# Optimization experiments

Hardware: AMD Instinct MI355X
Metric: run time of the kernel (lower is better)

Reference implementation:

```python
import jax, jax.numpy as jnp
import numpy as np

EMBED = 1024
HEADS = 16


def setup_inputs() -> dict:
    key = jax.random.key(0)
    ks = jax.random.split(key, 12)
    B, S, E = 8, 4096, EMBED
    img = jax.random.normal(ks[0], (B, S, E), dtype=jnp.float32)
    text = jax.random.normal(ks[1], (B, 1, E), dtype=jnp.float32)
    scale = 0.02
    W_kit = jax.random.normal(ks[2], (E, E), dtype=jnp.float32) * scale
    b_kit = jnp.zeros((E,), jnp.float32)
    W_vit = jax.random.normal(ks[3], (E, E), dtype=jnp.float32) * scale
    b_vit = jnp.zeros((E,), jnp.float32)
    W_kti = jax.random.normal(ks[4], (E, E), dtype=jnp.float32) * scale
    b_kti = jnp.zeros((E,), jnp.float32)
    W_vti = jax.random.normal(ks[5], (E, E), dtype=jnp.float32) * scale
    b_vti = jnp.zeros((E,), jnp.float32)
    W_out = jax.random.normal(ks[6], (E, E), dtype=jnp.float32) * scale
    b_out = jnp.zeros((E,), jnp.float32)
    return {
        "img": img, "text": text,
        "W_kit": W_kit, "b_kit": b_kit,
        "W_vit": W_vit, "b_vit": b_vit,
        "W_kti": W_kti, "b_kti": b_kti,
        "W_vti": W_vti, "b_vti": b_vti,
        "W_out": W_out, "b_out": b_out,
        "num_heads": HEADS,
    }


def reference(img, text, W_kit, b_kit, W_vit, b_vit, W_kti, b_kti,
              W_vti, b_vti, W_out, b_out, num_heads):
    B, S, E = img.shape
    H = num_heads
    D = E // H
    inv_sqrt_d = 1.0 / jnp.sqrt(jnp.asarray(D, img.dtype))

    # Projections (torch Linear with weights stored as [in, out] here)
    k_it = (img @ W_kit + b_kit).reshape(B, S, H, D)   # img_to_text_keys
    v_it = (img @ W_vit + b_vit).reshape(B, S, H, D)   # img_to_text_values
    k_ti = (text @ W_kti + b_kti).reshape(B, 1, H, D)  # text_to_img_keys
    v_ti = (text @ W_vti + b_vti).reshape(B, 1, H, D)  # text_to_img_values

    # text.repeat(1, S, 1).view(B, S, H, D): text has seq len 1
    t_keys = jnp.broadcast_to(text, (B, S, E)).reshape(B, S, H, D)
    img_keys = img.reshape(B, S, H, D)

    # NOTE: the original einsums attend over the HEADS axis (q,k = H),
    # with n = sequence position. Attention matrices are [B, S, H, H].
    img_att = jax.nn.softmax(
        jnp.einsum('bnqd,bnkd->bnqk', t_keys, k_it) * inv_sqrt_d, axis=-1)
    # torch einsum broadcasts the size-1 'n' dim of k_ti; do it explicitly
    k_ti_b = jnp.broadcast_to(k_ti, (B, S, H, D))
    v_ti_b = jnp.broadcast_to(v_ti, (B, S, H, D))
    text_att = jax.nn.softmax(
        jnp.einsum('bnqd,bnkd->bnqk', img_keys, k_ti_b) * inv_sqrt_d, axis=-1)

    img_out = jnp.einsum('bnql,bnld->bnqd', img_att, v_it).reshape(B, S, E)
    text_out = jnp.einsum('bnql,bnld->bnqd', text_att, v_ti_b).reshape(B, S, E)

    out = jnp.concatenate((img_out, text_out), axis=1)  # [B, 2S, E]
    return out @ W_out + b_out
```

## Files before the change

kernel.cpp:

```cpp
#include <hip/hip_runtime.h>
#include <stdint.h>

#define E_DIM 1024
#define SEQ 4096
#define BATCH 8

typedef unsigned short u16;
typedef __attribute__((ext_vector_type(8))) short bf16x8;
typedef __attribute__((ext_vector_type(4))) float f32x4;

static __device__ __forceinline__ float bf2f(u16 u){
  union { unsigned u; float f; } x; x.u = ((unsigned)u) << 16; return x.f;
}
static __device__ __forceinline__ u16 f2bf(float f){
  union { float f; unsigned u; } x; x.f = f;
  unsigned r = (x.u + 0x7fffu + ((x.u >> 16) & 1u)) >> 16;
  return (u16)r;
}
static __device__ __forceinline__ void lds_fence(){
  __asm__ volatile("s_waitcnt lgkmcnt(0)" ::: "memory");
}
static __device__ __forceinline__ void gload_lds16(const u16* g, u16* l){
  __builtin_amdgcn_global_load_lds(
      (const __attribute__((address_space(1))) unsigned int*)g,
      (__attribute__((address_space(3))) unsigned int*)l, 16, 0, 0);
}

__global__ __launch_bounds__(256) void conv_f2b(
    const float* __restrict__ src, u16* __restrict__ dst)
{
  size_t i = ((size_t)blockIdx.x * 256 + threadIdx.x) * 8;
  float4 a = *(const float4*)(src + i);
  float4 b = *(const float4*)(src + i + 4);
  u16 tmp[8] __attribute__((aligned(16)));
  tmp[0] = f2bf(a.x); tmp[1] = f2bf(a.y); tmp[2] = f2bf(a.z); tmp[3] = f2bf(a.w);
  tmp[4] = f2bf(b.x); tmp[5] = f2bf(b.y); tmp[6] = f2bf(b.z); tmp[7] = f2bf(b.w);
  *(uint4*)(dst + i) = *(const uint4*)tmp;
}

__global__ __launch_bounds__(256) void prep_transpose(
    const float* __restrict__ Wkit, const float* __restrict__ Wvit,
    const float* __restrict__ Wout, u16* __restrict__ Wt_kv,
    u16* __restrict__ Wt_out)
{
  __shared__ __align__(16) float sT[64][65];
  int m = blockIdx.y;
  const float* src = (m == 0) ? Wkit : (m == 1) ? Wvit : Wout;
  u16* dst = (m == 0) ? Wt_kv : (m == 1) ? (Wt_kv + 1024 * 1024) : Wt_out;
  int tile = blockIdx.x;
  int r0 = (tile & 15) * 64;
  int c0 = (tile >> 4) * 64;
  int t = threadIdx.x;
  #pragma unroll
  for (int it = 0; it < 4; ++it){
    int idx = t + it * 256;
    int r = idx >> 4, cq = idx & 15;
    float4 v = *(const float4*)(src + (size_t)(r0 + r) * 1024 + c0 + cq * 4);
    sT[r][cq * 4 + 0] = v.x; sT[r][cq * 4 + 1] = v.y;
    sT[r][cq * 4 + 2] = v.z; sT[r][cq * 4 + 3] = v.w;
  }
  __syncthreads();
  #pragma unroll
  for (int it = 0; it < 2; ++it){
    int idx = t + it * 256;
    int c = idx >> 3, rb = idx & 7;
    u16 tmp[8] __attribute__((aligned(16)));
    #pragma unroll
    for (int j = 0; j < 8; ++j) tmp[j] = f2bf(sT[rb * 8 + j][c]);
    *(uint4*)(dst + (size_t)(c0 + c) * 1024 + r0 + rb * 8) = *(const uint4*)tmp;
  }
}

__global__ __launch_bounds__(256) void prep_bias(
    const float* __restrict__ bkit, const float* __restrict__ bvit,
    float* __restrict__ bkv)
{
  int i = blockIdx.x * 256 + threadIdx.x;
  bkv[i] = (i < 1024) ? bkit[i] : bvit[i - 1024];
}

__global__ __launch_bounds__(1024) void prep_ti(
    const float* __restrict__ text,
    const float* __restrict__ Wk, const float* __restrict__ bk,
    const float* __restrict__ Wv, const float* __restrict__ bv,
    u16* __restrict__ kti, u16* __restrict__ vtiT)
{
  __shared__ __align__(16) float sT[1024];
  int b = blockIdx.x;
  int m = blockIdx.y;
  int e = threadIdx.x;
  const float* W = (m == 0) ? Wk : Wv;
  const float* bias = (m == 0) ? bk : bv;
  sT[e] = text[(size_t)b * 1024 + e];
  __syncthreads();
  float acc = bias[e];
  #pragma unroll 8
  for (int k = 0; k < 1024; ++k)
    acc += sT[k] * W[(size_t)k * 1024 + e];
  u16 r = f2bf(acc);
  if (m == 0) kti[(size_t)b * 1024 + e] = r;
  else {
    int kh = e >> 6, d = e & 63;
    vtiT[(size_t)b * 1024 + d * 16 + kh] = r;
  }
}

template <typename CT, bool VPERM>
__global__ __launch_bounds__(256, 2) void gemm_bt(
    const u16* __restrict__ A, const u16* __restrict__ Bt,
    const float* __restrict__ bias, CT* __restrict__ C,
    int n_tiles, int G, int ldc)
{
  __shared__ __align__(16) u16 sA[128 * 64];
  __shared__ __align__(16) u16 sB[128 * 64];
  int nwg = gridDim.x;
  int cpx = nwg >> 3;
  int bid = (blockIdx.x & 7) * cpx + (blockIdx.x >> 3);
  int gb = G * n_tiles;
  int g = bid / gb;
  int r = bid - g * gb;
  int mt = g * G + (r % G);
  int nt = r / G;
  int m0 = mt * 128, n0 = nt * 128;
  int tid = threadIdx.x;
  int w = tid >> 6, lane = tid & 63;
  int wm = w & 1, wn = w >> 1;
  int quad = lane >> 4, l15 = lane & 15;
  f32x4 acc[4][4];
  #pragma unroll
  for (int i = 0; i < 4; ++i)
    #pragma unroll
    for (int j = 0; j < 4; ++j)
      acc[i][j] = (f32x4){0.f, 0.f, 0.f, 0.f};
  const u16* Abase = A + (size_t)m0 * 1024;
  const u16* Bbase = Bt + (size_t)n0 * 1024;
  int srow = lane >> 3;
  int scol = (lane & 7) * 8;
  for (int kt = 0; kt < 16; ++kt){
    int k0 = kt * 64;
    #pragma unroll
    for (int i = 0; i < 4; ++i){
      int c = i * 4 + w;
      int grow = c * 8 + srow;
      gload_lds16(Abase + (size_t)grow * 1024 + k0 + scol, sA + c * 512);
      gload_lds16(Bbase + (size_t)grow * 1024 + k0 + scol, sB + c * 512);
    }
    __syncthreads();
    #pragma unroll
    for (int ks = 0; ks < 2; ++ks){
      bf16x8 af[4], bfr[4];
      #pragma unroll
      for (int mi = 0; mi < 4; ++mi){
        int rt = wm * 64 + mi * 16 + l15;
        af[mi] = *(const bf16x8*)(sA + rt * 64 + (ks * 4 + quad) * 8);
      }
      #pragma unroll
      for (int ni = 0; ni < 4; ++ni){
        int rt = wn * 64 + ni * 16 + l15;
        bfr[ni] = *(const bf16x8*)(sB + rt * 64 + (ks * 4 + quad) * 8);
      }
      #pragma unroll
      for (int mi = 0; mi < 4; ++mi)
        #pragma unroll
        for (int ni = 0; ni < 4; ++ni)
          acc[mi][ni] = __builtin_amdgcn_mfma_f32_16x16x32_bf16(
              af[mi], bfr[ni], acc[mi][ni], 0, 0, 0);
    }
    __syncthreads();
  }
  #pragma unroll
  for (int ni = 0; ni < 4; ++ni){
    int col = n0 + wn * 64 + ni * 16 + l15;
    float bv = bias[col];
    #pragma unroll
    for (int mi = 0; mi < 4; ++mi){
      int row0 = m0 + wm * 64 + mi * 16 + quad * 4;
      #pragma unroll
      for (int rg = 0; rg < 4; ++rg){
        float v = acc[mi][ni][rg] + bv;
        size_t cidx;
        if constexpr (VPERM) {
          if (n0 >= 1024) {
            int c2 = col - 1024;
            cidx = (size_t)(row0 + rg) * ldc + 1024 + (c2 & 63) * 16 + (c2 >> 6);
          } else {
            cidx = (size_t)(row0 + rg) * ldc + col;
          }
        } else {
          cidx = (size_t)(row0 + rg) * ldc + col;
        }
        if constexpr (sizeof(CT) == 2)
          C[cidx] = (CT)f2bf(v);
        else
          C[cidx] = (CT)v;
      }
    }
  }
}

static __device__ __forceinline__ void softmax16(const f32x4& s, float* p){
  #pragma unroll
  for (int g = 0; g < 4; ++g){
    float v = s[g] * 0.125f;
    float m = v;
    m = fmaxf(m, __shfl_xor(m, 1, 16));
    m = fmaxf(m, __shfl_xor(m, 2, 16));
    m = fmaxf(m, __shfl_xor(m, 4, 16));
    m = fmaxf(m, __shfl_xor(m, 8, 16));
    float e = __expf(v - m);
    float t = e;
    t += __shfl_xor(t, 1, 16);
    t += __shfl_xor(t, 2, 16);
    t += __shfl_xor(t, 4, 16);
    t += __shfl_xor(t, 8, 16);
    p[g] = e / t;
  }
}

__global__ __launch_bounds__(256) void attn_kernel(
    const u16* __restrict__ img, const u16* __restrict__ text,
    const u16* __restrict__ kv, const u16* __restrict__ kti,
    const u16* __restrict__ vtiT, u16* __restrict__ attn, int b0)
{
  __shared__ __align__(16) u16 sP[4][16 * 32];
  int tid = threadIdx.x;
  int w = tid >> 6, lane = tid & 63;
  int quad = lane >> 4, l15 = lane & 15;
  u16* sPw = sP[w];
  const f32x4 fz = {0.f, 0.f, 0.f, 0.f};
  const bf16x8 bz = {0, 0, 0, 0, 0, 0, 0, 0};
  int rloc = blockIdx.x * 4 + w;
  int bb = rloc >> 12;
  int n = rloc & 4095;
  int b = b0 + bb;
  const u16* xrow = img + ((size_t)b * SEQ + n) * E_DIM;
  const u16* trow = text + (size_t)b * E_DIM;
  const u16* kvrow = kv + (size_t)rloc * 2048;
  u16* dst1 = attn + ((size_t)bb * 8192 + n) * E_DIM;
  u16* dst2 = attn + ((size_t)bb * 8192 + 4096 + n) * E_DIM;

  {
    f32x4 s = fz;
    #pragma unroll
    for (int ks = 0; ks < 2; ++ks){
      bf16x8 a  = *(const bf16x8*)(trow  + l15 * 64 + ks * 32 + quad * 8);
      bf16x8 bk = *(const bf16x8*)(kvrow + l15 * 64 + ks * 32 + quad * 8);
      s = __builtin_amdgcn_mfma_f32_16x16x32_bf16(a, bk, s, 0, 0, 0);
    }
    float p[4];
    softmax16(s, p);
    #pragma unroll
    for (int g2 = 0; g2 < 4; ++g2)
      sPw[(quad * 4 + g2) * 32 + l15] = f2bf(p[g2]);
    lds_fence();
    bf16x8 aP = bz;
    if (quad < 2) aP = *(const bf16x8*)(sPw + l15 * 32 + quad * 8);
    const u16* vrow = kvrow + 1024;
    #pragma unroll
    for (int ni = 0; ni < 4; ++ni){
      bf16x8 bV = bz;
      if (quad < 2)
        bV = *(const bf16x8*)(vrow + (ni * 16 + l15) * 16 + quad * 8);
      f32x4 o = __builtin_amdgcn_mfma_f32_16x16x32_bf16(aP, bV, fz, 0, 0, 0);
      #pragma unroll
      for (int g2 = 0; g2 < 4; ++g2)
        dst1[(quad * 4 + g2) * 64 + ni * 16 + l15] = f2bf(o[g2]);
    }
  }
  {
    const u16* ktib = kti + (size_t)b * E_DIM;
    const u16* vtb  = vtiT + (size_t)b * E_DIM;
    f32x4 s = fz;
    #pragma unroll
    for (int ks = 0; ks < 2; ++ks){
      bf16x8 a  = *(const bf16x8*)(xrow + l15 * 64 + ks * 32 + quad * 8);
      bf16x8 bk = *(const bf16x8*)(ktib + l15 * 64 + ks * 32 + quad * 8);
      s = __builtin_amdgcn_mfma_f32_16x16x32_bf16(a, bk, s, 0, 0, 0);
    }
    float p[4];
    softmax16(s, p);
    lds_fence();
    #pragma unroll
    for (int g2 = 0; g2 < 4; ++g2)
      sPw[(quad * 4 + g2) * 32 + l15] = f2bf(p[g2]);
    lds_fence();
    bf16x8 aP = bz;
    if (quad < 2) aP = *(const bf16x8*)(sPw + l15 * 32 + quad * 8);
    #pragma unroll
    for (int ni = 0; ni < 4; ++ni){
      bf16x8 bV = bz;
      if (quad < 2)
        bV = *(const bf16x8*)(vtb + (ni * 16 + l15) * 16 + quad * 8);
      f32x4 o = __builtin_amdgcn_mfma_f32_16x16x32_bf16(aP, bV, fz, 0, 0, 0);
      #pragma unroll
      for (int g2 = 0; g2 < 4; ++g2)
        dst2[(quad * 4 + g2) * 64 + ni * 16 + l15] = f2bf(o[g2]);
    }
  }
}

extern "C" void kernel_launch(void* const* d_in, const int* in_sizes, int n_in,
                              void* d_out, int out_size, void* d_ws, size_t ws_size,
                              hipStream_t stream) {
  const float* img  = (const float*)d_in[0];
  const float* text = (const float*)d_in[1];
  const float* Wkit = (const float*)d_in[2];
  const float* bkit = (const float*)d_in[3];
  const float* Wvit = (const float*)d_in[4];
  const float* bvit = (const float*)d_in[5];
  const float* Wkti = (const float*)d_in[6];
  const float* bkti = (const float*)d_in[7];
  const float* Wvti = (const float*)d_in[8];
  const float* bvti = (const float*)d_in[9];
  const float* Wout = (const float*)d_in[10];
  const float* bout = (const float*)d_in[11];
  float* out = (float*)d_out;

  u16* wsp    = (u16*)d_ws;
  u16* Wt_kv  = wsp;
  u16* Wt_out = Wt_kv + 2048 * 1024;
  u16* kti    = Wt_out + 1024 * 1024;
  u16* vtiT   = kti + 8 * 1024;
  u16* tb16   = vtiT + 8 * 1024;
  u16* imgb   = tb16 + 8 * 1024;
  float* bkv  = (float*)(imgb + (size_t)BATCH * SEQ * E_DIM);
  u16* cbuf   = (u16*)(bkv + 2048);

  size_t prefix_bytes = (size_t)((u16*)cbuf - wsp) * 2;
  size_t full_need = prefix_bytes +
      ((size_t)BATCH * SEQ * 2048 + (size_t)BATCH * 2 * SEQ * 1024) * 2;
  int CH = (ws_size >= full_need) ? BATCH : 1;
  int nc = BATCH / CH;

  conv_f2b<<<(BATCH * SEQ * E_DIM) / (256 * 8), 256, 0, stream>>>(img, imgb);
  conv_f2b<<<(BATCH * E_DIM) / (256 * 8), 256, 0, stream>>>(text, tb16);
  prep_transpose<<<dim3(256, 3), 256, 0, stream>>>(Wkit, Wvit, Wout, Wt_kv, Wt_out);
  prep_bias<<<8, 256, 0, stream>>>(bkit, bvit, bkv);
  prep_ti<<<dim3(8, 2), 1024, 0, stream>>>(text, Wkti, bkti, Wvti, bvti, kti, vtiT);

  for (int c = 0; c < nc; ++c){
    int b0 = c * CH;
    int rows = CH * SEQ;
    u16* kvb = cbuf;
    u16* attnb = cbuf + (size_t)rows * 2048;
    int mt1 = rows / 128, nt1 = 16;
    gemm_bt<u16, true><<<mt1 * nt1, 256, 0, stream>>>(
        imgb + (size_t)b0 * SEQ * E_DIM, Wt_kv, bkv, kvb, nt1, 8, 2048);
    attn_kernel<<<rows / 4, 256, 0, stream>>>(imgb, tb16, kvb, kti, vtiT, attnb, b0);
    int mt2 = rows * 2 / 128, nt2 = 8;
    gemm_bt<float, false><<<mt2 * nt2, 256, 0, stream>>>(
        attnb, Wt_out, bout, out + (size_t)b0 * 2 * SEQ * E_DIM, nt2, 8, 1024);
  }
}
```

Measured before the change: 914.5 us.

## Replace 128x128 GEMM with 256x256 tile, 8-wave pipelined swizzled-LDS kernel

Replaces the 128x128 bf16 MFMA GEMM with a 256x256 tile kernel using 512 threads and a double-buffered 128KB LDS layout. Global-to-LDS loads for the next k-steps are interleaved with four MFMA quadrants, fenced by explicit vmcnt/lgkmcnt waits, barriers and setprio. The LDS layout is XOR-swizzled to avoid bank conflicts. The goal is to cut load stalls and raise arithmetic intensity for both projection GEMMs, at the cost of more registers, fewer tiles per device and complex hand-scheduled synchronisation.

Measured after the change: 904.7 us. About the same (-1.1%).

```diff
diff --git a/kernel.cpp b/kernel.cpp
--- a/kernel.cpp
+++ b/kernel.cpp
@@ -25,6 +25,14 @@
       (const __attribute__((address_space(1))) unsigned int*)g,
       (__attribute__((address_space(3))) unsigned int*)l, 16, 0, 0);
 }
+
+#define BAR()   __builtin_amdgcn_s_barrier()
+#define SCHED0  __builtin_amdgcn_sched_barrier(0)
+#define PRIO1   __builtin_amdgcn_s_setprio(1)
+#define PRIO0   __builtin_amdgcn_s_setprio(0)
+#define WAIT_LGKM0() do { asm volatile("s_waitcnt lgkmcnt(0)" ::: "memory"); SCHED0; } while (0)
+#define WAIT_VM6()   do { asm volatile("s_waitcnt vmcnt(6)" ::: "memory"); SCHED0; } while (0)
+#define WAIT_VM0()   do { asm volatile("s_waitcnt vmcnt(0)" ::: "memory"); SCHED0; } while (0)
 
 __global__ __launch_bounds__(256) void conv_f2b(
     const float* __restrict__ src, u16* __restrict__ dst)
@@ -105,14 +113,31 @@
   }
 }
 
+#define MFMA_Q(MIH, NIH) do { \
+  _Pragma("unroll") \
+  for (int mi_ = 0; mi_ < 4; ++mi_) { \
+    _Pragma("unroll") \
+    for (int ni_ = 0; ni_ < 2; ++ni_) { \
+      acc[(MIH)*4+mi_][(NIH)*2+ni_] = __builtin_amdgcn_mfma_f32_16x16x32_bf16( \
+          a[(MIH)*4+mi_][0], b[(NIH)*2+ni_][0], acc[(MIH)*4+mi_][(NIH)*2+ni_], 0, 0, 0); \
+      acc[(MIH)*4+mi_][(NIH)*2+ni_] = __builtin_amdgcn_mfma_f32_16x16x32_bf16( \
+          a[(MIH)*4+mi_][1], b[(NIH)*2+ni_][1], acc[(MIH)*4+mi_][(NIH)*2+ni_], 0, 0, 0); \
+    } \
+  } \
+} while (0)
+
+#define STAGE_HALF(GB, LB) do { \
+  gload_lds16((GB) + sP0, (LB) + (w * 2 + 0) * 512); \
+  gload_lds16((GB) + sP1, (LB) + (w * 2 + 1) * 512); \
+} while (0)
+
 template <typename CT, bool VPERM>
-__global__ __launch_bounds__(256, 2) void gemm_bt(
+__global__ __launch_bounds__(512, 2) void gemm256(
     const u16* __restrict__ A, const u16* __restrict__ Bt,
     const float* __restrict__ bias, CT* __restrict__ C,
     int n_tiles, int G, int ldc)
 {
-  __shared__ __align__(16) u16 sA[128 * 64];
-  __shared__ __align__(16) u16 sB[128 * 64];
+  __shared__ __align__(16) u16 lds[65536];
   int nwg = gridDim.x;
   int cpx = nwg >> 3;
   int bid = (blockIdx.x & 7) * cpx + (blockIdx.x >> 3);
@@ -121,60 +146,111 @@
   int r = bid - g * gb;
   int mt = g * G + (r % G);
   int nt = r / G;
-  int m0 = mt * 128, n0 = nt * 128;
+  int m0 = mt * 256, n0 = nt * 256;
   int tid = threadIdx.x;
   int w = tid >> 6, lane = tid & 63;
-  int wm = w & 1, wn = w >> 1;
+  int wm = w >> 2, wn = w & 3;
   int quad = lane >> 4, l15 = lane & 15;
-  f32x4 acc[4][4];
+
+  const u16* Ab = A + (size_t)m0 * 1024;
+  const u16* Bb = Bt + (size_t)n0 * 1024;
+
+  int i0 = (w * 2 + 0) * 64 + lane;
+  int i1 = (w * 2 + 1) * 64 + lane;
+  int r0s = i0 >> 3, r1s = i1 >> 3;
+  int sP0 = r0s * 1024 + (((i0 & 7) ^ (r0s & 7)) * 8);
+  int sP1 = r1s * 1024 + (((i1 & 7) ^ (r1s & 7)) * 8);
+
+  int swz0 = ((0 * 4 + quad) ^ (l15 & 7)) * 8;
+  int swz1 = ((1 * 4 + quad) ^ (l15 & 7)) * 8;
+  int ra0 = wm * 128 + l15;
+  int rb0 = wn * 64 + l15;
+  int aoff0 = ra0 * 64 + swz0, aoff1 = ra0 * 64 + swz1;
+  int boff0 = rb0 * 64 + swz0, boff1 = rb0 * 64 + swz1;
+
+  f32x4 acc[8][4];
   #pragma unroll
-  for (int i = 0; i < 4; ++i)
+  for (int i = 0; i < 8; ++i)
     #pragma unroll
     for (int j = 0; j < 4; ++j)
       acc[i][j] = (f32x4){0.f, 0.f, 0.f, 0.f};
-  const u16* Abase = A + (size_t)m0 * 1024;
-  const u16* Bbase = Bt + (size_t)n0 * 1024;
-  int srow = lane >> 3;
-  int scol = (lane & 7) * 8;
-  for (int kt = 0; kt < 16; ++kt){
-    int k0 = kt * 64;
-    #pragma unroll
-    for (int i = 0; i < 4; ++i){
-      int c = i * 4 + w;
-      int grow = c * 8 + srow;
-      gload_lds16(Abase + (size_t)grow * 1024 + k0 + scol, sA + c * 512);
-      gload_lds16(Bbase + (size_t)grow * 1024 + k0 + scol, sB + c * 512);
-    }
-    __syncthreads();
-    #pragma unroll
-    for (int ks = 0; ks < 2; ++ks){
-      bf16x8 af[4], bfr[4];
+
+  STAGE_HALF(Ab + 0,           lds + 0);
+  STAGE_HALF(Ab + 131072,      lds + 8192);
+  STAGE_HALF(Bb + 0,           lds + 32768);
+  STAGE_HALF(Bb + 131072,      lds + 32768 + 8192);
+  STAGE_HALF(Ab + 64,          lds + 16384);
+  STAGE_HALF(Ab + 131072 + 64, lds + 16384 + 8192);
+  STAGE_HALF(Bb + 64,          lds + 32768 + 16384);
+  WAIT_VM6();
+  BAR(); SCHED0;
+
+  #pragma unroll 2
+  for (int k = 0; k < 16; ++k){
+    const int c = k & 1, cn = c ^ 1;
+    const u16* pa = lds + c * 16384;
+    const u16* pb = lds + 32768 + c * 16384;
+    bf16x8 a[8][2], b[4][2];
+    if (wm == 0){
+      #pragma unroll
+      for (int mi = 0; mi < 8; ++mi){
+        a[mi][0] = *(const bf16x8*)(pa + aoff0 + mi * 1024);
+        a[mi][1] = *(const bf16x8*)(pa + aoff1 + mi * 1024);
+      }
+    } else {
       #pragma unroll
       for (int mi = 0; mi < 4; ++mi){
-        int rt = wm * 64 + mi * 16 + l15;
-        af[mi] = *(const bf16x8*)(sA + rt * 64 + (ks * 4 + quad) * 8);
+        a[mi][0] = *(const bf16x8*)(pa + aoff0 + mi * 1024);
+        a[mi][1] = *(const bf16x8*)(pa + aoff1 + mi * 1024);
       }
-      #pragma unroll
-      for (int ni = 0; ni < 4; ++ni){
-        int rt = wn * 64 + ni * 16 + l15;
-        bfr[ni] = *(const bf16x8*)(sB + rt * 64 + (ks * 4 + quad) * 8);
+    }
+    #pragma unroll
+    for (int ni = 0; ni < 2; ++ni){
+      b[ni][0] = *(const bf16x8*)(pb + boff0 + ni * 1024);
+      b[ni][1] = *(const bf16x8*)(pb + boff1 + ni * 1024);
+    }
+    if (k + 1 < 16)
+      STAGE_HALF(Bb + 131072 + (k + 1) * 64, lds + 32768 + cn * 16384 + 8192);
+    WAIT_LGKM0();
+    BAR(); SCHED0;
+    PRIO1; MFMA_Q(0, 0); PRIO0;
+    BAR(); SCHED0;
+    if (wm == 1){
+      #pragma unroll
+      for (int mi = 4; mi < 8; ++mi){
+        a[mi][0] = *(const bf16x8*)(pa + aoff0 + mi * 1024);
+        a[mi][1] = *(const bf16x8*)(pa + aoff1 + mi * 1024);
       }
-      #pragma unroll
-      for (int mi = 0; mi < 4; ++mi)
-        #pragma unroll
-        for (int ni = 0; ni < 4; ++ni)
-          acc[mi][ni] = __builtin_amdgcn_mfma_f32_16x16x32_bf16(
-              af[mi], bfr[ni], acc[mi][ni], 0, 0, 0);
-    }
-    __syncthreads();
-  }
+    }
+    #pragma unroll
+    for (int ni = 2; ni < 4; ++ni){
+      b[ni][0] = *(const bf16x8*)(pb + boff0 + ni * 1024);
+      b[ni][1] = *(const bf16x8*)(pb + boff1 + ni * 1024);
+    }
+    if (k + 2 < 16)
+      STAGE_HALF(Ab + (k + 2) * 64, lds + c * 16384);
+    WAIT_LGKM0();
+    BAR(); SCHED0;
+    PRIO1; MFMA_Q(0, 1); PRIO0;
+    BAR(); SCHED0;
+    if (k + 2 < 16)
+      STAGE_HALF(Ab + 131072 + (k + 2) * 64, lds + c * 16384 + 8192);
+    PRIO1; MFMA_Q(1, 0); PRIO0;
+    BAR(); SCHED0;
+    if (k + 2 < 16)
+      STAGE_HALF(Bb + (k + 2) * 64, lds + 32768 + c * 16384);
+    if (k < 14) { WAIT_VM6(); } else { WAIT_VM0(); }
+    BAR(); SCHED0;
+    PRIO1; MFMA_Q(1, 1); PRIO0;
+  }
+
   #pragma unroll
   for (int ni = 0; ni < 4; ++ni){
     int col = n0 + wn * 64 + ni * 16 + l15;
     float bv = bias[col];
     #pragma unroll
-    for (int mi = 0; mi < 4; ++mi){
-      int row0 = m0 + wm * 64 + mi * 16 + quad * 4;
+    for (int mi = 0; mi < 8; ++mi){
+      int row0 = m0 + wm * 128 + mi * 16 + quad * 4;
       #pragma unroll
       for (int rg = 0; rg < 4; ++rg){
         float v = acc[mi][ni][rg] + bv;
@@ -343,12 +419,12 @@
     int rows = CH * SEQ;
     u16* kvb = cbuf;
     u16* attnb = cbuf + (size_t)rows * 2048;
-    int mt1 = rows / 128, nt1 = 16;
-    gemm_bt<u16, true><<<mt1 * nt1, 256, 0, stream>>>(
+    int mt1 = rows / 256, nt1 = 8;
+    gemm256<u16, true><<<mt1 * nt1, 512, 0, stream>>>(
         imgb + (size_t)b0 * SEQ * E_DIM, Wt_kv, bkv, kvb, nt1, 8, 2048);
     attn_kernel<<<rows / 4, 256, 0, stream>>>(imgb, tb16, kvb, kti, vtiT, attnb, b0);
-    int mt2 = rows * 2 / 128, nt2 = 8;
-    gemm_bt<float, false><<<mt2 * nt2, 256, 0, stream>>>(
+    int mt2 = rows * 2 / 256, nt2 = 4;
+    gemm256<float, false><<<mt2 * nt2, 512, 0, stream>>>(
         attnb, Wt_out, bout, out + (size_t)b0 * 2 * SEQ * E_DIM, nt2, 8, 1024);
   }
 }
```
